# Optimization experiments

Measured on AMD Instinct MI355X. Metric: run time of the kernel, lower is better.

Reference implementation:

```python
import math
import jax, jax.numpy as jnp
import numpy as np

B, T, D = 8, 2048, 512


def setup_inputs() -> dict:
    key = jax.random.key(0)
    kx, = jax.random.split(key, 1)
    x = jax.random.normal(kx, (B, T, D), dtype=jnp.float32)
    log_tau = jnp.asarray(math.log(2.0), dtype=jnp.float32)
    log_blend = jnp.asarray(math.log(0.3 / 0.7), dtype=jnp.float32)
    return {"x": x, "log_tau": log_tau, "log_blend": log_blend}


def _gelu_tanh(x):
    c = math.sqrt(2.0 / math.pi)
    return 0.5 * x * (1.0 + jnp.tanh(c * (x + 0.044715 * x * x * x)))


def reference(x, log_tau, log_blend):
    Bb, Tt, Dd = x.shape
    tau = jnp.exp(log_tau)
    alpha = jax.nn.sigmoid(log_blend)
    # F.normalize(x, dim=-1): divide by L2 norm clamped to eps=1e-12
    norm = jnp.maximum(jnp.linalg.norm(x, axis=-1, keepdims=True), 1e-12)
    x_norm = x / norm
    # cosine self-similarity [B, T, T]
    sim = jnp.einsum("btd,bsd->bts", x_norm, x_norm)
    # triu(diagonal=0) masks j >= i (current + future positions)
    causal_mask = jnp.triu(jnp.ones((Tt, Tt), dtype=bool), k=0)
    sim_causal = jnp.where(causal_mask[None, :, :], -jnp.inf, sim)
    max_sim = jnp.max(sim_causal, axis=-1)  # [B, T]; row 0 is -inf
    max_sim = jnp.nan_to_num(max_sim, nan=0.0, posinf=1.0, neginf=-1.0)
    novelty = jnp.exp(-tau * max_sim)
    scale = (1.0 - alpha + alpha * novelty)[..., None]  # [B, T, 1]
    return _gelu_tanh(x * scale)
```

## Files before the change

### kernel.cpp

```cpp
#include <hip/hip_runtime.h>

#define B_ 8
#define T_ 2048
#define D_ 512

typedef float f32x16 __attribute__((ext_vector_type(16)));
typedef __bf16 bf16x8 __attribute__((ext_vector_type(8)));

__device__ __forceinline__ unsigned encf(float f) {
    int i = __float_as_int(f);
    return (i < 0) ? ~((unsigned)i) : (((unsigned)i) | 0x80000000u);
}
__device__ __forceinline__ float decf(unsigned u) {
    unsigned b = (u & 0x80000000u) ? (u ^ 0x80000000u) : ~u;
    return __int_as_float((int)b);
}

__device__ __forceinline__ void gload_lds16(const char* g, char* l) {
    __builtin_amdgcn_global_load_lds(
        (const __attribute__((address_space(1))) unsigned int*)g,
        (__attribute__((address_space(3))) unsigned int*)l, 16, 0, 0);
}

__global__ __launch_bounds__(256) void pack_kernel(
        const float* __restrict__ x, char* __restrict__ xnp,
        unsigned* __restrict__ msim, float* __restrict__ rnorm) {
    __shared__ __attribute__((aligned(16))) char sP[32768];
    int blk = blockIdx.x;
    int t   = threadIdx.x;
    int ln  = t & 63, w = t >> 6;

#pragma unroll
    for (int q = 0; q < 8; q++) {
        int row32 = q * 4 + w;
        const float* p = x + ((size_t)blk * 32 + row32) * D_ + ln * 8;
        float4 a = *(const float4*)p;
        float4 c = *(const float4*)(p + 4);
        float ss = a.x*a.x + a.y*a.y + a.z*a.z + a.w*a.w
                 + c.x*c.x + c.y*c.y + c.z*c.z + c.w*c.w;
#pragma unroll
        for (int m = 32; m; m >>= 1) ss += __shfl_xor(ss, m);
        if (ln == 0)
            rnorm[blk * 32 + row32] = 1.0f / fmaxf(sqrtf(ss), 1e-12f);
        bf16x8 h;
        h[0] = (__bf16)a.x; h[1] = (__bf16)a.y;
        h[2] = (__bf16)a.z; h[3] = (__bf16)a.w;
        h[4] = (__bf16)c.x; h[5] = (__bf16)c.y;
        h[6] = (__bf16)c.z; h[7] = (__bf16)c.w;
        int ks = ln >> 1, hcw = ln & 1;
        int slot = row32 + hcw * 32;
        int off = ks * 1024 + ((slot * 16) ^ ((ks & 7) << 4));
        *(bf16x8*)(sP + off) = h;
    }
    if (t < 32) msim[blk * 32 + t] = encf(-1e30f);
    __syncthreads();
#pragma unroll
    for (int iq = 0; iq < 8; iq++) {
        int beta = iq * 4096 + t * 16;
        int ks = beta >> 10;
        bf16x8 v = *(const bf16x8*)(sP + ks * 1024 +
                     ((beta & 1023) ^ ((ks & 7) << 4)));
        *(bf16x8*)(xnp + (size_t)blk * 32768 + beta) = v;
    }
}

__global__ __launch_bounds__(512, 1) void simmax_kernel(
        const char* __restrict__ xnp, const float* __restrict__ rnorm,
        unsigned* __restrict__ msim) {
    __shared__ __attribute__((aligned(16))) char sB[131072];

    int bid = blockIdx.x;
    int b   = bid & 7;
    int u   = bid >> 3;
    int j, c;
    if (u >= 64) {
        int p = u - 64; j = 2 * p + 1; c = 7 - p;
    } else {
        j = 0; int acc = 0;
        while (acc + ((16 - j) >> 1) <= u) { acc += (16 - j) >> 1; j++; }
        c = u - acc;
    }
    int c0  = j * 128;
    int rp0 = c0 + c * 256;

    int t  = threadIdx.x;
    int ln = t & 63, w = t >> 6;
    int lr = ln & 31, hc = ln >> 5;
    const float NINF = -__builtin_inff();

    const char* gB = xnp + (size_t)(b * 64 + j * 4) * 32768;
#pragma unroll
    for (int q = 0; q < 16; q++) {
        int L = w * 16 + q;
        gload_lds16(gB + L * 1024 + ln * 16, sB + L * 1024 + ln * 16);
    }
    __syncthreads();

    int myr = rp0 + 32 * w;
    if (myr < T_) {
        const char* gA = xnp + (size_t)(b * 64 + (myr >> 5)) * 32768 + ln * 16;
        const char* lB = sB + ln * 16;
        f32x16 a0, a1, a2, a3;
#pragma unroll
        for (int r = 0; r < 16; r++) { a0[r]=0.f; a1[r]=0.f; a2[r]=0.f; a3[r]=0.f; }

#pragma unroll 8
        for (int k = 0; k < 32; k++) {
            bf16x8 av = *(const bf16x8*)(gA + k * 1024);
            bf16x8 b0 = *(const bf16x8*)(lB +          k * 1024);
            bf16x8 b1 = *(const bf16x8*)(lB + 32768  + k * 1024);
            bf16x8 b2 = *(const bf16x8*)(lB + 65536  + k * 1024);
            bf16x8 b3 = *(const bf16x8*)(lB + 98304  + k * 1024);
            a0 = __builtin_amdgcn_mfma_f32_32x32x16_bf16(av, b0, a0, 0, 0, 0);
            a1 = __builtin_amdgcn_mfma_f32_32x32x16_bf16(av, b1, a1, 0, 0, 0);
            a2 = __builtin_amdgcn_mfma_f32_32x32x16_bf16(av, b2, a2, 0, 0, 0);
            a3 = __builtin_amdgcn_mfma_f32_32x32x16_bf16(av, b3, a3, 0, 0, 0);
        }

        const float* rnc = rnorm + b * T_;
        float rn0 = rnc[c0 + lr],      rn1 = rnc[c0 + 32 + lr];
        float rn2 = rnc[c0 + 64 + lr], rn3 = rnc[c0 + 96 + lr];
        bool dt = (c0 + 127 >= myr);
        unsigned* mrow = msim + (size_t)b * T_ + myr;
#pragma unroll
        for (int r = 0; r < 16; r++) {
            int crow = (r & 3) + 8 * (r >> 2) + 4 * hc;
            int row  = myr + crow;
            float t0 = a0[r] * rn0, t1 = a1[r] * rn1;
            float t2 = a2[r] * rn2, t3 = a3[r] * rn3;
            if (dt) {
                if (c0 + lr      >= row) t0 = NINF;
                if (c0 + 32 + lr >= row) t1 = NINF;
                if (c0 + 64 + lr >= row) t2 = NINF;
                if (c0 + 96 + lr >= row) t3 = NINF;
            }
            float v = fmaxf(fmaxf(t0, t1), fmaxf(t2, t3));
            v = fmaxf(v, __shfl_xor(v, 1));
            v = fmaxf(v, __shfl_xor(v, 2));
            v = fmaxf(v, __shfl_xor(v, 4));
            v = fmaxf(v, __shfl_xor(v, 8));
            v = fmaxf(v, __shfl_xor(v, 16));
            if (lr == 0) atomicMax(&mrow[crow], encf(v));
        }
    }
}

__global__ __launch_bounds__(256) void gelu_kernel(
        const float* __restrict__ x, const unsigned* __restrict__ msim,
        const float* __restrict__ rnorm,
        const float* __restrict__ ltau, const float* __restrict__ lblend,
        float* __restrict__ out) {
    int i = blockIdx.x * 256 + threadIdx.x;
    float tau   = __expf(ltau[0]);
    float alpha = 1.f / (1.f + __expf(-lblend[0]));
    int row = i >> 7;
    float raw = decf(msim[row]);
    float ms  = (raw < -1e29f) ? -1.0f : raw * rnorm[row];
    float sc = (1.f - alpha) + alpha * __expf(-tau * ms);
    float4 v = ((const float4*)x)[i];
    const float c0 = 0.7978845608028654f;
    const float c1 = 0.044715f;
    float4 o;
#pragma unroll
    for (int k = 0; k < 4; k++) {
        float z = ((const float*)&v)[k] * sc;
        float u = c0 * (z + c1 * z * z * z);
        float e = __expf(2.f * u);
        float th = 1.f - 2.f / (e + 1.f);
        ((float*)&o)[k] = 0.5f * z * (1.f + th);
    }
    ((float4*)out)[i] = o;
}

extern "C" void kernel_launch(void* const* d_in, const int* in_sizes, int n_in,
                              void* d_out, int out_size, void* d_ws, size_t ws_size,
                              hipStream_t stream) {
    (void)in_sizes; (void)n_in; (void)out_size; (void)ws_size;
    const float* x      = (const float*)d_in[0];
    const float* ltau   = (const float*)d_in[1];
    const float* lblend = (const float*)d_in[2];
    float*    out   = (float*)d_out;
    char*     xnp   = (char*)d_out;
    unsigned* msim  = (unsigned*)d_ws;
    float*    rnorm = (float*)((char*)d_ws + 65536);

    pack_kernel<<<B_ * T_ / 32, 256, 0, stream>>>(x, xnp, msim, rnorm);
    simmax_kernel<<<B_ * 72, 512, 0, stream>>>(xnp, rnorm, msim);
    gelu_kernel<<<(B_ * T_ * D_ / 4) / 256, 256, 0, stream>>>(
        x, msim, rnorm, ltau, lblend, out);
}
```

Baseline: 66.32 us.

## Retile simmax to 64x64 warp tiles with smaller LDS and software-pipelined loads

The similarity-max kernel changes from 32-row × 128-column warp tiles to 64×64 tiles. Each warp now loads two A row-blocks from global memory and two B column-blocks from a halved 64KB LDS buffer. The loads are double-buffered so the next k-step's fragments are fetched while the current MFMAs run. A new block-to-tile mapping covers the causal triangle with 80 blocks per batch, and launch bounds allow 4 blocks per CU so latency is better hidden. The risks are higher register pressure from the prefetch buffers and twice as many global A reads per warp.

```diff
diff --git a/kernel.cpp b/kernel.cpp
--- a/kernel.cpp
+++ b/kernel.cpp
@@ -64,83 +64,110 @@
     }
 }
 
-__global__ __launch_bounds__(512, 1) void simmax_kernel(
+__global__ __launch_bounds__(512, 4) void simmax_kernel(
         const char* __restrict__ xnp, const float* __restrict__ rnorm,
         unsigned* __restrict__ msim) {
-    __shared__ __attribute__((aligned(16))) char sB[131072];
+    __shared__ __attribute__((aligned(16))) char sB[65536];
 
     int bid = blockIdx.x;
     int b   = bid & 7;
     int u   = bid >> 3;
     int j, c;
-    if (u >= 64) {
-        int p = u - 64; j = 2 * p + 1; c = 7 - p;
-    } else {
-        j = 0; int acc = 0;
-        while (acc + ((16 - j) >> 1) <= u) { acc += (16 - j) >> 1; j++; }
-        c = u - acc;
-    }
-    int c0  = j * 128;
-    int rp0 = c0 + c * 256;
+    if (u < 32)      { j = u >> 2;            c = u & 3; }
+    else if (u < 56) { j = 8 + (u - 32) / 3;  c = (u - 32) % 3; }
+    else if (u < 72) { j = 16 + ((u - 56) >> 1); c = (u - 56) & 1; }
+    else             { j = 24 + (u - 72);     c = 0; }
+    int Cj   = (39 - j) >> 3;
+    int row0 = T_ - 512 * (Cj - c);
 
     int t  = threadIdx.x;
     int ln = t & 63, w = t >> 6;
     int lr = ln & 31, hc = ln >> 5;
     const float NINF = -__builtin_inff();
 
-    const char* gB = xnp + (size_t)(b * 64 + j * 4) * 32768;
-#pragma unroll
-    for (int q = 0; q < 16; q++) {
-        int L = w * 16 + q;
+    const char* gB = xnp + (size_t)(b * 64 + 2 * j) * 32768;
+#pragma unroll
+    for (int q = 0; q < 8; q++) {
+        int L = w * 8 + q;
         gload_lds16(gB + L * 1024 + ln * 16, sB + L * 1024 + ln * 16);
     }
     __syncthreads();
 
-    int myr = rp0 + 32 * w;
-    if (myr < T_) {
+    int myr = row0 + 64 * w;
+    if (64 * j < myr + 63) {
         const char* gA = xnp + (size_t)(b * 64 + (myr >> 5)) * 32768 + ln * 16;
         const char* lB = sB + ln * 16;
-        f32x16 a0, a1, a2, a3;
-#pragma unroll
-        for (int r = 0; r < 16; r++) { a0[r]=0.f; a1[r]=0.f; a2[r]=0.f; a3[r]=0.f; }
-
-#pragma unroll 8
-        for (int k = 0; k < 32; k++) {
-            bf16x8 av = *(const bf16x8*)(gA + k * 1024);
-            bf16x8 b0 = *(const bf16x8*)(lB +          k * 1024);
-            bf16x8 b1 = *(const bf16x8*)(lB + 32768  + k * 1024);
-            bf16x8 b2 = *(const bf16x8*)(lB + 65536  + k * 1024);
-            bf16x8 b3 = *(const bf16x8*)(lB + 98304  + k * 1024);
-            a0 = __builtin_amdgcn_mfma_f32_32x32x16_bf16(av, b0, a0, 0, 0, 0);
-            a1 = __builtin_amdgcn_mfma_f32_32x32x16_bf16(av, b1, a1, 0, 0, 0);
-            a2 = __builtin_amdgcn_mfma_f32_32x32x16_bf16(av, b2, a2, 0, 0, 0);
-            a3 = __builtin_amdgcn_mfma_f32_32x32x16_bf16(av, b3, a3, 0, 0, 0);
+
+        f32x16 c00, c01, c10, c11;
+#pragma unroll
+        for (int r = 0; r < 16; r++) {
+            c00[r] = 0.f; c01[r] = 0.f; c10[r] = 0.f; c11[r] = 0.f;
         }
 
+        bf16x8 pa0, pa1, pb0, pb1, qa0, qa1, qb0, qb1;
+#define LOADS(s, k) do {                                                    \
+    s##a0 = *(const bf16x8*)(gA +         (k) * 1024);                      \
+    s##a1 = *(const bf16x8*)(gA + 32768 + (k) * 1024);                      \
+    s##b0 = *(const bf16x8*)(lB +         (k) * 1024);                      \
+    s##b1 = *(const bf16x8*)(lB + 32768 + (k) * 1024);                      \
+} while (0)
+#define MM(s) do {                                                          \
+    c00 = __builtin_amdgcn_mfma_f32_32x32x16_bf16(s##a0, s##b0, c00, 0,0,0);\
+    c01 = __builtin_amdgcn_mfma_f32_32x32x16_bf16(s##a0, s##b1, c01, 0,0,0);\
+    c10 = __builtin_amdgcn_mfma_f32_32x32x16_bf16(s##a1, s##b0, c10, 0,0,0);\
+    c11 = __builtin_amdgcn_mfma_f32_32x32x16_bf16(s##a1, s##b1, c11, 0,0,0);\
+} while (0)
+
+        LOADS(p, 0);
+        LOADS(q, 1);
+#pragma unroll
+        for (int k = 0; k < 32; k += 2) {
+            MM(p);
+            if (k + 2 < 32) LOADS(p, k + 2);
+            MM(q);
+            if (k + 3 < 32) LOADS(q, k + 3);
+        }
+#undef LOADS
+#undef MM
+
         const float* rnc = rnorm + b * T_;
-        float rn0 = rnc[c0 + lr],      rn1 = rnc[c0 + 32 + lr];
-        float rn2 = rnc[c0 + 64 + lr], rn3 = rnc[c0 + 96 + lr];
-        bool dt = (c0 + 127 >= myr);
+        float rn0 = rnc[64 * j + lr];
+        float rn1 = rnc[64 * j + 32 + lr];
+        bool strad = (64 * j + 63 >= myr);
         unsigned* mrow = msim + (size_t)b * T_ + myr;
 #pragma unroll
         for (int r = 0; r < 16; r++) {
             int crow = (r & 3) + 8 * (r >> 2) + 4 * hc;
-            int row  = myr + crow;
-            float t0 = a0[r] * rn0, t1 = a1[r] * rn1;
-            float t2 = a2[r] * rn2, t3 = a3[r] * rn3;
-            if (dt) {
-                if (c0 + lr      >= row) t0 = NINF;
-                if (c0 + 32 + lr >= row) t1 = NINF;
-                if (c0 + 64 + lr >= row) t2 = NINF;
-                if (c0 + 96 + lr >= row) t3 = NINF;
+            {
+                int row = myr + crow;
+                float t0 = c00[r] * rn0, t1 = c01[r] * rn1;
+                if (strad) {
+                    if (64 * j + lr      >= row) t0 = NINF;
+                    if (64 * j + 32 + lr >= row) t1 = NINF;
+                }
+                float v = fmaxf(t0, t1);
+                v = fmaxf(v, __shfl_xor(v, 1));
+                v = fmaxf(v, __shfl_xor(v, 2));
+                v = fmaxf(v, __shfl_xor(v, 4));
+                v = fmaxf(v, __shfl_xor(v, 8));
+                v = fmaxf(v, __shfl_xor(v, 16));
+                if (lr == 0) atomicMax(&mrow[crow], encf(v));
             }
-            float v = fmaxf(fmaxf(t0, t1), fmaxf(t2, t3));
-            v = fmaxf(v, __shfl_xor(v, 1));
-            v = fmaxf(v, __shfl_xor(v, 2));
-            v = fmaxf(v, __shfl_xor(v, 4));
-            v = fmaxf(v, __shfl_xor(v, 8));
-            v = fmaxf(v, __shfl_xor(v, 16));
-            if (lr == 0) atomicMax(&mrow[crow], encf(v));
+            {
+                int row = myr + 32 + crow;
+                float t0 = c10[r] * rn0, t1 = c11[r] * rn1;
+                if (strad) {
+                    if (64 * j + lr      >= row) t0 = NINF;
+                    if (64 * j + 32 + lr >= row) t1 = NINF;
+                }
+                float v = fmaxf(t0, t1);
+                v = fmaxf(v, __shfl_xor(v, 1));
+                v = fmaxf(v, __shfl_xor(v, 2));
+                v = fmaxf(v, __shfl_xor(v, 4));
+                v = fmaxf(v, __shfl_xor(v, 8));
+                v = fmaxf(v, __shfl_xor(v, 16));
+                if (lr == 0) atomicMax(&mrow[32 + crow], encf(v));
+            }
         }
     }
 }
@@ -185,7 +212,7 @@
     float*    rnorm = (float*)((char*)d_ws + 65536);
 
     pack_kernel<<<B_ * T_ / 32, 256, 0, stream>>>(x, xnp, msim, rnorm);
-    simmax_kernel<<<B_ * 72, 512, 0, stream>>>(xnp, rnorm, msim);
+    simmax_kernel<<<B_ * 80, 512, 0, stream>>>(xnp, rnorm, msim);
     gelu_kernel<<<(B_ * T_ * D_ / 4) / 256, 256, 0, stream>>>(
         x, msim, rnorm, ltau, lblend, out);
 }
```

New measurement: 70.03 us. +5.6%, slower.
